# Optimization experiments

Measured on AMD Instinct MI355X. Metric: run time of the kernel, lower is better.

Reference implementation:

```python
import jax, jax.numpy as jnp
import numpy as np

LN2 = 0.6931471805599453

def ssp(x):
    # 'shifted_sp' activation: softplus(x) - log(2)
    return jax.nn.softplus(x) - LN2

def _res_chain(x, W1, b1, W2, b2):
    # PhysNetResidual chain: x <- lin2(ssp(lin1(ssp(x)))) + x
    # W1/W2: [n_res, F, F], b1/b2: [n_res, F]
    for j in range(W1.shape[0]):
        h = ssp(x) @ W1[j] + b1[j]
        x = ssp(h) @ W2[j] + b2[j] + x
    return x

def _physnet_module(feat, radial_aev, idx12, p):
    (W_I, b_I, W_J, b_J, W_gate, gvec, W_int, b_int,
     ri_W1, ri_b1, ri_W2, ri_b2,
     ra_W1, ra_b1, ra_W2, ra_b2,
     ro_W1, ro_b1, ro_W2, ro_b2, W_out, b_out) = p
    N, F = feat.shape
    # self term (no species are dummy -> non_dummy indexing is identity)
    h_self = ssp(ssp(feat) @ W_I + b_I)                       # [N,F]
    # pair messages
    gate = radial_aev @ W_gate                                 # [P,F] (no bias)
    f12 = feat[idx12]                                          # [2,P,F] gather
    fm = ssp(ssp(f12) @ W_J + b_J)                             # [2,P,F]
    pair_msg = gate[None] * fm                                 # [2,P,F]
    proto = jnp.zeros_like(feat).at[idx12.reshape(-1)].add(
        pair_msg.reshape(-1, F))                               # scatter-add
    proto = proto + h_self
    msg = _res_chain(proto, ri_W1, ri_b1, ri_W2, ri_b2)
    feat2 = feat * gvec + ssp(msg) @ W_int + b_int
    feat2 = _res_chain(feat2, ra_W1, ra_b1, ra_W2, ra_b2)
    e = ssp(_res_chain(feat2, ro_W1, ro_b1, ro_W2, ro_b2)) @ W_out + b_out  # [N]
    return e, feat2

def setup_inputs() -> dict:
    key = jax.random.key(0)
    L, F, R = 5, 128, 64
    M, A = 128, 64
    N = M * A
    P = 400000
    ks = jax.random.split(key, 20)
    s = 0.05  # small weight scale keeps activations stable across 5 modules
    inp = {
        'species': jax.random.randint(ks[0], (M, A), 0, 4, dtype=jnp.int32),
        'features': jax.random.normal(ks[1], (N, F), jnp.float32),
        'radial_aev': jax.random.uniform(ks[2], (P, R), jnp.float32),
        'atom_index12': jax.random.randint(ks[3], (2, P), 0, N, dtype=jnp.int32),
        'W_I': jax.random.normal(ks[4], (L, F, F)) * s,
        'b_I': jnp.zeros((L, F)),
        'W_J': jax.random.normal(ks[5], (L, F, F)) * s,
        'b_J': jnp.zeros((L, F)),
        'W_gate': jax.random.normal(ks[6], (L, R, F)) * s,
        'gvec': jnp.ones((L, F)),
        'W_int': jax.random.normal(ks[7], (L, F, F)) * s,
        'b_int': jnp.zeros((L, F)),
        'ri_W1': jax.random.normal(ks[8], (L, 3, F, F)) * s,
        'ri_b1': jnp.zeros((L, 3, F)),
        'ri_W2': jax.random.normal(ks[9], (L, 3, F, F)) * s,
        'ri_b2': jnp.zeros((L, 3, F)),
        'ra_W1': jax.random.normal(ks[10], (L, 2, F, F)) * s,
        'ra_b1': jnp.zeros((L, 2, F)),
        'ra_W2': jax.random.normal(ks[11], (L, 2, F, F)) * s,
        'ra_b2': jnp.zeros((L, 2, F)),
        'ro_W1': jax.random.normal(ks[12], (L, 1, F, F)) * s,
        'ro_b1': jnp.zeros((L, 1, F)),
        'ro_W2': jax.random.normal(ks[13], (L, 1, F, F)) * s,
        'ro_b2': jnp.zeros((L, 1, F)),
        'W_out': jax.random.normal(ks[14], (L, F)) * s,
        'b_out': jnp.zeros((L,)),
    }
    return inp

def reference(species, features, radial_aev, atom_index12,
              W_I, b_I, W_J, b_J, W_gate, gvec, W_int, b_int,
              ri_W1, ri_b1, ri_W2, ri_b2,
              ra_W1, ra_b1, ra_W2, ra_b2,
              ro_W1, ro_b1, ro_W2, ro_b2, W_out, b_out):
    M, A = species.shape
    params = (W_I, b_I, W_J, b_J, W_gate, gvec, W_int, b_int,
              ri_W1, ri_b1, ri_W2, ri_b2,
              ra_W1, ra_b1, ra_W2, ra_b2,
              ro_W1, ro_b1, ro_W2, ro_b2, W_out, b_out)
    feat = features
    energies = jnp.zeros((M * A,), features.dtype)
    for l in range(W_I.shape[0]):  # fixed small module loop
        p = tuple(arr[l] for arr in params)
        e, feat = _physnet_module(feat, radial_aev, atom_index12, p)
        energies = energies + e
    return energies.reshape(M, A), feat
```

## Files before the change

### kernel.cpp

```cpp
#include <hip/hip_runtime.h>


#define LN2F 0.69314718055994530942f
#define L2EF 1.44269504088896340736f
#define NB 128

using short8  = __attribute__((ext_vector_type(8))) short;
using float4v = __attribute__((ext_vector_type(4))) float;

__device__ __forceinline__ float sspf(float x) {
  float t = exp2f(-L2EF * fabsf(x));
  float l = log2f(1.0f + t);
  return fmaxf(x, 0.0f) + fmaf(LN2F, l, -LN2F);
}

__device__ __forceinline__ unsigned short f2bf(float x) {
  return (unsigned short)((__float_as_uint(x) + 0x8000u) >> 16);
}

__device__ __forceinline__ unsigned short f2bf_ne(float x) {
  unsigned int u = __float_as_uint(x);
  u += 0x7fffu + ((u >> 16) & 1u);
  return (unsigned short)(u >> 16);
}

struct K1Args {
  const float* wsrc[80];
  int isgate[80];
  const float* bp[17];
  int bstride[17];
  const float* b_out;
  const int* idx;
  unsigned short* Wt;
  float* bias_pack;
  unsigned int* H;
  int n2p, C;
};

__global__ __launch_bounds__(256) void k1_prep(K1Args K) {
  __shared__ unsigned int h[8192];
  int b = blockIdx.x, tid = threadIdx.x;
  if (b < 80) {
    const float* s = K.wsrc[b];
    unsigned short* d = K.Wt + (size_t)b * 16384;
    if (!K.isgate[b]) {
      for (int it = 0; it < 8; ++it) {
        int id = tid + it * 256;
        int lane = id & 63, mm = (id >> 6) & 3, c8 = id >> 8;
        int l16 = lane & 15, quad = lane >> 4;
        int n = 16 * c8 + l16, k0 = 8 * (4 * mm + quad);
        unsigned short tmp[8];
#pragma unroll
        for (int cc = 0; cc < 8; ++cc) tmp[cc] = f2bf_ne(s[(k0 + cc) * 128 + n]);
        *(uint4*)(d + c8 * 2048 + mm * 512 + lane * 8) = *(uint4*)tmp;
      }
    } else {
      for (int it = 0; it < 4; ++it) {
        int id = tid + it * 256;
        int lane = id & 63, mm = (id >> 6) & 1, c8 = id >> 7;
        int l16 = lane & 15, quad = lane >> 4;
        int n = 16 * c8 + l16, k0 = 8 * (4 * mm + quad);
        unsigned short tmp[8];
#pragma unroll
        for (int cc = 0; cc < 8; ++cc) tmp[cc] = f2bf_ne(s[(k0 + cc) * 128 + n]);
        *(uint4*)(d + c8 * 1024 + mm * 512 + lane * 8) = *(uint4*)tmp;
      }
    }
  } else if (b < 85) {
    int l = b - 80;
    for (int i = tid; i < 17 * 128; i += 256) {
      int s = i >> 7;
      K.bias_pack[(size_t)l * 2304 + i] = K.bp[s][l * K.bstride[s] + (i & 127)];
    }
    if (tid == 0) K.bias_pack[(size_t)l * 2304 + 17 * 128] = K.b_out[l];
  } else {
    int blk = b - 85;
    for (int i = tid; i < 8192; i += 256) h[i] = 0;
    __syncthreads();
    int s = blk * K.C, e = min(s + K.C, K.n2p);
    for (int i = s + tid; i < e; i += 256) atomicAdd(&h[K.idx[i]], 1u);
    __syncthreads();
    for (int i = tid; i < 8192; i += 256) K.H[(size_t)blk * 8192 + i] = h[i];
  }
}

__global__ __launch_bounds__(256) void col_scan(unsigned int* __restrict__ H,
                                                unsigned int* __restrict__ tot) {
  __shared__ unsigned int part[8][33];
  int c = threadIdx.x & 31, r8 = threadIdx.x >> 5;
  int col = blockIdx.x * 32 + c;
  unsigned int psum = 0;
#pragma unroll 4
  for (int r = r8 * 16; r < r8 * 16 + 16; ++r)
    psum += H[(size_t)r * 8192 + col];
  part[r8][c] = psum;
  __syncthreads();
  if (threadIdx.x < 32) {
    unsigned int run = 0;
#pragma unroll
    for (int s = 0; s < 8; ++s) {
      unsigned int v = part[s][threadIdx.x];
      part[s][threadIdx.x] = run;
      run += v;
    }
    tot[blockIdx.x * 32 + threadIdx.x] = run;
  }
  __syncthreads();
  unsigned int run = part[r8][c];
#pragma unroll 4
  for (int r = r8 * 16; r < r8 * 16 + 16; ++r) {
    unsigned int v = H[(size_t)r * 8192 + col];
    H[(size_t)r * 8192 + col] = run;
    run += v;
  }
}

__global__ __launch_bounds__(256) void place_pass(const int* __restrict__ idx,
                                                  const unsigned int* __restrict__ H,
                                                  const unsigned int* __restrict__ tot,
                                                  unsigned int* __restrict__ off_out,
                                                  unsigned int* __restrict__ pairid,
                                                  int P, int C) {
  __shared__ unsigned int pos[8192];
  __shared__ unsigned int wt4[4];
  int b = blockIdx.x, tid = threadIdx.x;
  unsigned int local[32], s = 0;
#pragma unroll
  for (int i = 0; i < 32; ++i) { local[i] = tot[tid * 32 + i]; s += local[i]; }
  unsigned int v = s;
  int lane = tid & 63, wv = tid >> 6;
#pragma unroll
  for (int o = 1; o < 64; o <<= 1) {
    unsigned int u = __shfl_up(v, o, 64);
    if (lane >= o) v += u;
  }
  if (lane == 63) wt4[wv] = v;
  __syncthreads();
  unsigned int base = 0;
  for (int k = 0; k < wv; ++k) base += wt4[k];
  unsigned int excl = base + v - s;
#pragma unroll
  for (int i = 0; i < 32; ++i) {
    pos[tid * 32 + i] = excl;
    if (b == 0) off_out[tid * 32 + i] = excl;
    excl += local[i];
  }
  if (b == 0 && tid == 255) off_out[8192] = excl;
  __syncthreads();
  for (int i = tid; i < 8192; i += 256) pos[i] += H[(size_t)b * 8192 + i];
  __syncthreads();
  int n2p = 2 * P;
  int s2 = b * C, e2 = min(s2 + C, n2p);
  for (int i = s2 + tid; i < e2; i += 256) {
    int a = idx[i];
    unsigned int p = atomicAdd(&pos[a], 1u);
    pairid[p] = (i >= P) ? (unsigned int)(i - P) : (unsigned int)i;
  }
}

__global__ __launch_bounds__(256) void gather_kernel(const float* __restrict__ radial,
                                                     const unsigned int* __restrict__ off,
                                                     const unsigned int* __restrict__ pairid,
                                                     float* __restrict__ S) {
  __shared__ float4v red[3][16];
  int a = blockIdx.x;
  int lane = threadIdx.x & 63, w = threadIdx.x >> 6;
  int grp = lane >> 4, l16v = lane & 15;
  unsigned int b = off[a], e = off[a + 1];
  float4v acc = {0.f, 0.f, 0.f, 0.f};
  for (unsigned int base = b; base < e; base += 128) {
    unsigned int pp[8];
#pragma unroll
    for (int k = 0; k < 8; ++k) {
      unsigned int j = base + k * 16 + w * 4 + grp;
      pp[k] = pairid[j < e ? j : b];
    }
    float4v vv[8];
#pragma unroll
    for (int k = 0; k < 8; ++k)
      vv[k] = *(const float4v*)(radial + (size_t)pp[k] * 64 + l16v * 4);
#pragma unroll
    for (int k = 0; k < 8; ++k) {
      unsigned int j = base + k * 16 + w * 4 + grp;
      if (j < e) acc += vv[k];
    }
  }
#pragma unroll
  for (int o = 16; o < 64; o <<= 1) {
#pragma unroll
    for (int cc = 0; cc < 4; ++cc) acc[cc] += __shfl_xor(acc[cc], o, 64);
  }
  if (w > 0 && grp == 0) red[w - 1][l16v] = acc;
  __syncthreads();
  if (w == 0 && grp == 0) {
    acc += red[0][l16v];
    acc += red[1][l16v];
    acc += red[2][l16v];
    *(float4v*)(S + (size_t)a * 64 + l16v * 4) = acc;
  }
}

struct ChainArgs {
  const float* feat_in;
  const float* S;
  const unsigned short* wt;
  const float* bias_pack;
  float* feat_out;
  float* energy;
};

#define MFMA_ __builtin_amdgcn_mfma_f32_16x16x32_bf16
#define APOFF 2176

#define BAR() { __builtin_amdgcn_sched_barrier(0); \
  asm volatile("s_waitcnt lgkmcnt(0)" ::: "memory"); \
  __builtin_amdgcn_s_barrier(); \
  __builtin_amdgcn_sched_barrier(0); }

#define LDW(WP, sp) { \
  const unsigned short* wp_ = (sp) + woff; \
  W[WP][0] = *(const short8*)(wp_); \
  W[WP][1] = *(const short8*)(wp_ + 512); \
  W[WP][2] = *(const short8*)(wp_ + 1024); \
  W[WP][3] = *(const short8*)(wp_ + 1536); }

#define BINI(ACC, B) { (ACC)[0] = (B); (ACC)[1] = (B); (ACC)[2] = (B); (ACC)[3] = (B); }

#define G128R(AP, WP, ACC) { \
  short8 a0_ = *(const short8*)(aB + (AP)*APOFF); \
  short8 a1_ = *(const short8*)(aB + (AP)*APOFF + 32); \
  short8 a2_ = *(const short8*)(aB + (AP)*APOFF + 64); \
  short8 a3_ = *(const short8*)(aB + (AP)*APOFF + 96); \
  ACC = MFMA_(a0_, W[WP][0], ACC, 0, 0, 0); \
  ACC = MFMA_(a1_, W[WP][1], ACC, 0, 0, 0); \
  ACC = MFMA_(a2_, W[WP][2], ACC, 0, 0, 0); \
  ACC = MFMA_(a3_, W[WP][3], ACC, 0, 0, 0); }

#define WSSPM(AP, V) { \
  float s0_ = sspf((V)[0]), s1_ = sspf((V)[1]); \
  float s2_ = sspf((V)[2]), s3_ = sspf((V)[3]); \
  unsigned int p01_, p23_; \
  asm("v_cvt_pk_bf16_f32 %0, %1, %2" : "=v"(p01_) : "v"(s0_), "v"(s1_)); \
  asm("v_cvt_pk_bf16_f32 %0, %1, %2" : "=v"(p23_) : "v"(s2_), "v"(s3_)); \
  wB[(AP)*APOFF]       = (unsigned short)p01_; \
  wB[(AP)*APOFF + 136] = (unsigned short)(p01_ >> 16); \
  wB[(AP)*APOFF + 272] = (unsigned short)p23_; \
  wB[(AP)*APOFF + 408] = (unsigned short)(p23_ >> 16); }

#define MODBODY(L, S0) { \
  const float* bp = A.bias_pack + (L) * 2304; \
  const unsigned short* wtp = A.wt + (size_t)(L) * 16 * 16384; \
  float bW[15]; \
  _Pragma("unroll") \
  for (int q = 0; q < 15; ++q) bW[q] = bp[q * 128 + col0]; \
  float gvv = bp[15 * 128 + col0], wvv = bp[16 * 128 + col0]; \
   \
  { LDW((S0)^1, wtp + 2*16384); \
    gG = Z; \
    { short8 s0_ = *(const short8*)(aS); short8 s1_ = *(const short8*)(aS + 32); \
      gG = MFMA_(s0_, GT0, gG, 0, 0, 0); \
      gG = MFMA_(s1_, GT1, gG, 0, 0, 0); } \
    BINI(fm, bW[0]); G128R(0, (S0), fm); \
    for (int r = 0; r < 4; ++r) fm[r] = sspf(fm[r]); } \
   \
  { LDW((S0), wtp + 3*16384); \
    if ((L) < 4) { \
      GT0 = *(const short8*)(wtp + 16*16384 + goff); \
      GT1 = *(const short8*)(wtp + 16*16384 + goff + 512); \
    } \
    BINI(t4, bW[1]); G128R(0, (S0)^1, t4); \
    for (int r = 0; r < 4; ++r) xf[r] = fm[r] * gG[r] + sspf(t4[r]); } \
  WSSPM(1, xf); BAR(); \
   \
  { LDW((S0)^1, wtp + 4*16384); BINI(t4, bW[2]); G128R(1, (S0), t4); } \
  WSSPM(0, t4); BAR(); \
  { LDW((S0), wtp + 5*16384); BINI(t4, bW[3]); G128R(0, (S0)^1, t4); \
    for (int r = 0; r < 4; ++r) xf[r] += t4[r]; } \
  WSSPM(1, xf); BAR(); \
  { LDW((S0)^1, wtp + 6*16384); BINI(t4, bW[4]); G128R(1, (S0), t4); } \
  WSSPM(0, t4); BAR(); \
  { LDW((S0), wtp + 7*16384); BINI(t4, bW[5]); G128R(0, (S0)^1, t4); \
    for (int r = 0; r < 4; ++r) xf[r] += t4[r]; } \
  WSSPM(1, xf); BAR(); \
  { LDW((S0)^1, wtp + 8*16384); BINI(t4, bW[6]); G128R(1, (S0), t4); } \
  WSSPM(0, t4); BAR(); \
  { LDW((S0), wtp + 9*16384); BINI(t4, bW[7]); G128R(0, (S0)^1, t4); \
    for (int r = 0; r < 4; ++r) xf[r] += t4[r]; } \
  WSSPM(1, xf); BAR(); \
   \
  { LDW((S0)^1, wtp + 10*16384); BINI(t4, bW[8]); G128R(1, (S0), t4); \
    for (int r = 0; r < 4; ++r) xf[r] = ff[r] * gvv + t4[r]; } \
  WSSPM(0, xf); BAR(); \
   \
  { LDW((S0), wtp + 11*16384); BINI(t4, bW[9]); G128R(0, (S0)^1, t4); } \
  WSSPM(1, t4); BAR(); \
  { LDW((S0)^1, wtp + 12*16384); BINI(t4, bW[10]); G128R(1, (S0), t4); \
    for (int r = 0; r < 4; ++r) xf[r] += t4[r]; } \
  WSSPM(0, xf); BAR(); \
  { LDW((S0), wtp + 13*16384); BINI(t4, bW[11]); G128R(0, (S0)^1, t4); } \
  WSSPM(1, t4); BAR(); \
  { LDW((S0)^1, wtp + 14*16384); BINI(t4, bW[12]); G128R(1, (S0), t4); \
    for (int r = 0; r < 4; ++r) xf[r] += t4[r]; } \
  WSSPM(0, xf); BAR(); \
  ff = xf; \
  if ((L) == 4) { \
    for (int r = 0; r < 4; ++r) \
      A.feat_out[(size_t)(row0 + quad*4 + r) * 128 + col0] = xf[r]; \
  } \
   \
  { LDW((S0), wtp + 15*16384); BINI(t4, bW[13]); G128R(0, (S0)^1, t4); } \
  WSSPM(1, t4); BAR(); \
   \
  { if ((L) < 4) LDW((S0)^1, wtp + 17*16384); \
    BINI(t4, bW[14]); G128R(1, (S0), t4); \
    p0 += sspf(xf[0] + t4[0]) * wvv; \
    p1 += sspf(xf[1] + t4[1]) * wvv; \
    p2 += sspf(xf[2] + t4[2]) * wvv; \
    p3 += sspf(xf[3] + t4[3]) * wvv; } \
  bsum += bp[17*128]; \
  BAR(); }

__global__ __launch_bounds__(512)
__attribute__((amdgpu_waves_per_eu(4, 4)))
void chain_kernel(ChainArgs A) {
  __shared__ __align__(16) unsigned short sA[2][16 * 136];
  __shared__ __align__(16) unsigned short sS[16 * 72];
  __shared__ float sE[16];

  const int tid  = threadIdx.x;
  const int row0 = blockIdx.x * 16;
  const int lane = tid & 63;
  const int c    = tid >> 6;
  const int l16  = lane & 15;
  const int quad = lane >> 4;
  const int col0 = 16 * c + l16;

  const int woff = c * 2048 + lane * 8;
  const int goff = c * 1024 + lane * 8;

  const unsigned short* aB = &sA[0][0] + l16 * 136 + quad * 8;
  unsigned short*       wB = &sA[0][0] + (quad * 4) * 136 + col0;
  const unsigned short* aS = &sS[0] + l16 * 72 + quad * 8;

  short8 GT0, GT1;
  short8 W[2][4];
  GT0 = *(const short8*)(A.wt + goff);
  GT1 = *(const short8*)(A.wt + goff + 512);
  LDW(0, A.wt + 16384);

  for (int i = tid; i < 16 * 64; i += 512) {
    int r = i >> 6, k = i & 63;
    sS[r * 72 + k] = f2bf(A.S[(size_t)(row0 + r) * 64 + k]);
  }
  for (int i = tid; i < 16 * 128; i += 512) {
    int r = i >> 7, k = i & 127;
    sA[0][r * 136 + k] = f2bf(sspf(A.feat_in[(size_t)(row0 + r) * 128 + k]));
  }
  float4v ff;
#pragma unroll
  for (int r = 0; r < 4; ++r)
    ff[r] = A.feat_in[(size_t)(row0 + quad * 4 + r) * 128 + col0];
  if (tid < 16) sE[tid] = 0.0f;
  __syncthreads();

  const float4v Z = {0.f, 0.f, 0.f, 0.f};
  float4v gG, fm, xf, t4;
  float p0 = 0.f, p1 = 0.f, p2 = 0.f, p3 = 0.f, bsum = 0.f;

  MODBODY(0, 0)
  MODBODY(1, 1)
  MODBODY(2, 0)
  MODBODY(3, 1)
  MODBODY(4, 0)

#pragma unroll
  for (int o = 1; o < 16; o <<= 1) {
    p0 += __shfl_xor(p0, o, 64);
    p1 += __shfl_xor(p1, o, 64);
    p2 += __shfl_xor(p2, o, 64);
    p3 += __shfl_xor(p3, o, 64);
  }
  if (l16 == 0) {
    atomicAdd(&sE[quad * 4 + 0], p0);
    atomicAdd(&sE[quad * 4 + 1], p1);
    atomicAdd(&sE[quad * 4 + 2], p2);
    atomicAdd(&sE[quad * 4 + 3], p3);
  }
  BAR();
  if (tid < 16) A.energy[row0 + tid] = sE[tid] + bsum;
}

extern "C" void kernel_launch(void* const* d_in, const int* in_sizes, int n_in,
                              void* d_out, int out_size, void* d_ws, size_t ws_size,
                              hipStream_t stream) {
  const float* features = (const float*)d_in[1];
  const float* radial   = (const float*)d_in[2];
  const int*   idx12    = (const int*)  d_in[3];
  const float* W_I    = (const float*)d_in[4];
  const float* b_I    = (const float*)d_in[5];
  const float* W_J    = (const float*)d_in[6];
  const float* b_J    = (const float*)d_in[7];
  const float* W_gate = (const float*)d_in[8];
  const float* gvec   = (const float*)d_in[9];
  const float* W_int  = (const float*)d_in[10];
  const float* b_int  = (const float*)d_in[11];
  const float* ri_W1  = (const float*)d_in[12];
  const float* ri_b1  = (const float*)d_in[13];
  const float* ri_W2  = (const float*)d_in[14];
  const float* ri_b2  = (const float*)d_in[15];
  const float* ra_W1  = (const float*)d_in[16];
  const float* ra_b1  = (const float*)d_in[17];
  const float* ra_W2  = (const float*)d_in[18];
  const float* ra_b2  = (const float*)d_in[19];
  const float* ro_W1  = (const float*)d_in[20];
  const float* ro_b1  = (const float*)d_in[21];
  const float* ro_W2  = (const float*)d_in[22];
  const float* ro_b2  = (const float*)d_in[23];
  const float* W_out  = (const float*)d_in[24];
  const float* b_out  = (const float*)d_in[25];

  const int N = in_sizes[1] / 128;
  const int P = in_sizes[3] / 2;
  const int L = in_sizes[25];
  const int n2p = 2 * P;
  const int C = (n2p + NB - 1) / NB;

  float* S = (float*)d_ws;
  float* bias_pack = S + (size_t)N * 64;
  unsigned short* Wt = (unsigned short*)(bias_pack + 5 * 2304);
  unsigned int* H      = (unsigned int*)(Wt + (size_t)80 * 16384);
  unsigned int* tot    = H + (size_t)NB * 8192;
  unsigned int* off    = tot + N;
  unsigned int* pairid = off + N + 4;

  K1Args k1;
  for (int l = 0; l < L; ++l) {
    const float* fx[16] = {
      W_gate + l * 8192,
      W_J + l * 16384, W_I + l * 16384,
      ri_W1 + (l * 3 + 0) * 16384, ri_W2 + (l * 3 + 0) * 16384,
      ri_W1 + (l * 3 + 1) * 16384, ri_W2 + (l * 3 + 1) * 16384,
      ri_W1 + (l * 3 + 2) * 16384, ri_W2 + (l * 3 + 2) * 16384,
      W_int + l * 16384,
      ra_W1 + (l * 2 + 0) * 16384, ra_W2 + (l * 2 + 0) * 16384,
      ra_W1 + (l * 2 + 1) * 16384, ra_W2 + (l * 2 + 1) * 16384,
      ro_W1 + l * 16384, ro_W2 + l * 16384 };
    for (int t = 0; t < 16; ++t) { k1.wsrc[l * 16 + t] = fx[t]; k1.isgate[l * 16 + t] = (t == 0); }
  }
  const float* bp[17] = { b_J, b_I,
    ri_b1, ri_b2, ri_b1 + 128, ri_b2 + 128, ri_b1 + 256, ri_b2 + 256,
    b_int, ra_b1, ra_b2, ra_b1 + 128, ra_b2 + 128, ro_b1, ro_b2, gvec, W_out };
  int st[17] = {128,128, 384,384,384,384,384,384, 128, 256,256,256,256, 128,128,128,128};
  for (int q = 0; q < 17; ++q) { k1.bp[q] = bp[q]; k1.bstride[q] = st[q]; }
  k1.b_out = b_out;
  k1.idx = idx12; k1.Wt = Wt; k1.bias_pack = bias_pack; k1.H = H;
  k1.n2p = n2p; k1.C = C;
  k1_prep<<<80 + 5 + NB, 256, 0, stream>>>(k1);

  col_scan<<<256, 256, 0, stream>>>(H, tot);
  place_pass<<<NB, 256, 0, stream>>>(idx12, H, tot, off, pairid, P, C);
  gather_kernel<<<N, 256, 0, stream>>>(radial, off, pairid, S);

  ChainArgs ca;
  ca.feat_in   = features;
  ca.S         = S;
  ca.wt        = Wt;
  ca.bias_pack = bias_pack;
  ca.energy    = (float*)d_out;
  ca.feat_out  = (float*)d_out + N;
  chain_kernel<<<N / 16, 512, 0, stream>>>(ca);
}
```

Baseline: 318.8 us.

## Process 32 rows per block in chain kernel to reuse weight registers

Each block of the chain kernel now handles two 16-row tiles instead of one. Every weight fragment loaded from global memory feeds two interleaved MFMA accumulators, which halves weight traffic per row and gives independent MFMA chains for latency hiding. The cost is double the LDS activation buffers, more registers per thread, waves-per-EU lowered from 4 to 2, and half as many blocks (256 instead of 512), which may underfill the GPU.

Result: slower. 327.1 us (+2.6%).

```diff
diff --git a/kernel.cpp b/kernel.cpp
--- a/kernel.cpp
+++ b/kernel.cpp
@@ -210,7 +210,8 @@
 };
 
 #define MFMA_ __builtin_amdgcn_mfma_f32_16x16x32_bf16
-#define APOFF 2176
+#define APOFF 4352
+#define TOFF  2176
 
 #define BAR() { __builtin_amdgcn_sched_barrier(0); \
   asm volatile("s_waitcnt lgkmcnt(0)" ::: "memory"); \
@@ -226,26 +227,36 @@
 
 #define BINI(ACC, B) { (ACC)[0] = (B); (ACC)[1] = (B); (ACC)[2] = (B); (ACC)[3] = (B); }
 
-#define G128R(AP, WP, ACC) { \
+#define G128R2(AP, WP, ACC0, ACC1) { \
   short8 a0_ = *(const short8*)(aB + (AP)*APOFF); \
   short8 a1_ = *(const short8*)(aB + (AP)*APOFF + 32); \
   short8 a2_ = *(const short8*)(aB + (AP)*APOFF + 64); \
   short8 a3_ = *(const short8*)(aB + (AP)*APOFF + 96); \
-  ACC = MFMA_(a0_, W[WP][0], ACC, 0, 0, 0); \
-  ACC = MFMA_(a1_, W[WP][1], ACC, 0, 0, 0); \
-  ACC = MFMA_(a2_, W[WP][2], ACC, 0, 0, 0); \
-  ACC = MFMA_(a3_, W[WP][3], ACC, 0, 0, 0); }
-
-#define WSSPM(AP, V) { \
+  short8 c0_ = *(const short8*)(aB2 + (AP)*APOFF); \
+  short8 c1_ = *(const short8*)(aB2 + (AP)*APOFF + 32); \
+  short8 c2_ = *(const short8*)(aB2 + (AP)*APOFF + 64); \
+  short8 c3_ = *(const short8*)(aB2 + (AP)*APOFF + 96); \
+  ACC0 = MFMA_(a0_, W[WP][0], ACC0, 0, 0, 0); \
+  ACC1 = MFMA_(c0_, W[WP][0], ACC1, 0, 0, 0); \
+  ACC0 = MFMA_(a1_, W[WP][1], ACC0, 0, 0, 0); \
+  ACC1 = MFMA_(c1_, W[WP][1], ACC1, 0, 0, 0); \
+  ACC0 = MFMA_(a2_, W[WP][2], ACC0, 0, 0, 0); \
+  ACC1 = MFMA_(c2_, W[WP][2], ACC1, 0, 0, 0); \
+  ACC0 = MFMA_(a3_, W[WP][3], ACC0, 0, 0, 0); \
+  ACC1 = MFMA_(c3_, W[WP][3], ACC1, 0, 0, 0); }
+
+#define WSSP_P(PTR, AP, V) { \
   float s0_ = sspf((V)[0]), s1_ = sspf((V)[1]); \
   float s2_ = sspf((V)[2]), s3_ = sspf((V)[3]); \
   unsigned int p01_, p23_; \
   asm("v_cvt_pk_bf16_f32 %0, %1, %2" : "=v"(p01_) : "v"(s0_), "v"(s1_)); \
   asm("v_cvt_pk_bf16_f32 %0, %1, %2" : "=v"(p23_) : "v"(s2_), "v"(s3_)); \
-  wB[(AP)*APOFF]       = (unsigned short)p01_; \
-  wB[(AP)*APOFF + 136] = (unsigned short)(p01_ >> 16); \
-  wB[(AP)*APOFF + 272] = (unsigned short)p23_; \
-  wB[(AP)*APOFF + 408] = (unsigned short)(p23_ >> 16); }
+  (PTR)[(AP)*APOFF]       = (unsigned short)p01_; \
+  (PTR)[(AP)*APOFF + 136] = (unsigned short)(p01_ >> 16); \
+  (PTR)[(AP)*APOFF + 272] = (unsigned short)p23_; \
+  (PTR)[(AP)*APOFF + 408] = (unsigned short)(p23_ >> 16); }
+
+#define WSSPM2(AP, V0, V1) { WSSP_P(wB, AP, V0); WSSP_P(wB2, AP, V1); }
 
 #define MODBODY(L, S0) { \
   const float* bp = A.bias_pack + (L) * 2304; \
@@ -256,79 +267,111 @@
   float gvv = bp[15 * 128 + col0], wvv = bp[16 * 128 + col0]; \
    \
   { LDW((S0)^1, wtp + 2*16384); \
-    gG = Z; \
+    gG0 = Z; gG1 = Z; \
     { short8 s0_ = *(const short8*)(aS); short8 s1_ = *(const short8*)(aS + 32); \
-      gG = MFMA_(s0_, GT0, gG, 0, 0, 0); \
-      gG = MFMA_(s1_, GT1, gG, 0, 0, 0); } \
-    BINI(fm, bW[0]); G128R(0, (S0), fm); \
-    for (int r = 0; r < 4; ++r) fm[r] = sspf(fm[r]); } \
+      short8 s2_ = *(const short8*)(aS2); short8 s3_ = *(const short8*)(aS2 + 32); \
+      gG0 = MFMA_(s0_, GT0, gG0, 0, 0, 0); \
+      gG1 = MFMA_(s2_, GT0, gG1, 0, 0, 0); \
+      gG0 = MFMA_(s1_, GT1, gG0, 0, 0, 0); \
+      gG1 = MFMA_(s3_, GT1, gG1, 0, 0, 0); } \
+    BINI(fm0, bW[0]); BINI(fm1, bW[0]); \
+    G128R2(0, (S0), fm0, fm1); \
+    for (int r = 0; r < 4; ++r) fm0[r] = sspf(fm0[r]); \
+    for (int r = 0; r < 4; ++r) fm1[r] = sspf(fm1[r]); } \
    \
   { LDW((S0), wtp + 3*16384); \
     if ((L) < 4) { \
       GT0 = *(const short8*)(wtp + 16*16384 + goff); \
       GT1 = *(const short8*)(wtp + 16*16384 + goff + 512); \
     } \
-    BINI(t4, bW[1]); G128R(0, (S0)^1, t4); \
-    for (int r = 0; r < 4; ++r) xf[r] = fm[r] * gG[r] + sspf(t4[r]); } \
-  WSSPM(1, xf); BAR(); \
-   \
-  { LDW((S0)^1, wtp + 4*16384); BINI(t4, bW[2]); G128R(1, (S0), t4); } \
-  WSSPM(0, t4); BAR(); \
-  { LDW((S0), wtp + 5*16384); BINI(t4, bW[3]); G128R(0, (S0)^1, t4); \
-    for (int r = 0; r < 4; ++r) xf[r] += t4[r]; } \
-  WSSPM(1, xf); BAR(); \
-  { LDW((S0)^1, wtp + 6*16384); BINI(t4, bW[4]); G128R(1, (S0), t4); } \
-  WSSPM(0, t4); BAR(); \
-  { LDW((S0), wtp + 7*16384); BINI(t4, bW[5]); G128R(0, (S0)^1, t4); \
-    for (int r = 0; r < 4; ++r) xf[r] += t4[r]; } \
-  WSSPM(1, xf); BAR(); \
-  { LDW((S0)^1, wtp + 8*16384); BINI(t4, bW[6]); G128R(1, (S0), t4); } \
-  WSSPM(0, t4); BAR(); \
-  { LDW((S0), wtp + 9*16384); BINI(t4, bW[7]); G128R(0, (S0)^1, t4); \
-    for (int r = 0; r < 4; ++r) xf[r] += t4[r]; } \
-  WSSPM(1, xf); BAR(); \
-   \
-  { LDW((S0)^1, wtp + 10*16384); BINI(t4, bW[8]); G128R(1, (S0), t4); \
-    for (int r = 0; r < 4; ++r) xf[r] = ff[r] * gvv + t4[r]; } \
-  WSSPM(0, xf); BAR(); \
-   \
-  { LDW((S0), wtp + 11*16384); BINI(t4, bW[9]); G128R(0, (S0)^1, t4); } \
-  WSSPM(1, t4); BAR(); \
-  { LDW((S0)^1, wtp + 12*16384); BINI(t4, bW[10]); G128R(1, (S0), t4); \
-    for (int r = 0; r < 4; ++r) xf[r] += t4[r]; } \
-  WSSPM(0, xf); BAR(); \
-  { LDW((S0), wtp + 13*16384); BINI(t4, bW[11]); G128R(0, (S0)^1, t4); } \
-  WSSPM(1, t4); BAR(); \
-  { LDW((S0)^1, wtp + 14*16384); BINI(t4, bW[12]); G128R(1, (S0), t4); \
-    for (int r = 0; r < 4; ++r) xf[r] += t4[r]; } \
-  WSSPM(0, xf); BAR(); \
-  ff = xf; \
+    BINI(t40, bW[1]); BINI(t41, bW[1]); \
+    G128R2(0, (S0)^1, t40, t41); \
+    for (int r = 0; r < 4; ++r) xf0[r] = fm0[r] * gG0[r] + sspf(t40[r]); \
+    for (int r = 0; r < 4; ++r) xf1[r] = fm1[r] * gG1[r] + sspf(t41[r]); } \
+  WSSPM2(1, xf0, xf1); BAR(); \
+   \
+  { LDW((S0)^1, wtp + 4*16384); BINI(t40, bW[2]); BINI(t41, bW[2]); \
+    G128R2(1, (S0), t40, t41); } \
+  WSSPM2(0, t40, t41); BAR(); \
+  { LDW((S0), wtp + 5*16384); BINI(t40, bW[3]); BINI(t41, bW[3]); \
+    G128R2(0, (S0)^1, t40, t41); \
+    for (int r = 0; r < 4; ++r) xf0[r] += t40[r]; \
+    for (int r = 0; r < 4; ++r) xf1[r] += t41[r]; } \
+  WSSPM2(1, xf0, xf1); BAR(); \
+  { LDW((S0)^1, wtp + 6*16384); BINI(t40, bW[4]); BINI(t41, bW[4]); \
+    G128R2(1, (S0), t40, t41); } \
+  WSSPM2(0, t40, t41); BAR(); \
+  { LDW((S0), wtp + 7*16384); BINI(t40, bW[5]); BINI(t41, bW[5]); \
+    G128R2(0, (S0)^1, t40, t41); \
+    for (int r = 0; r < 4; ++r) xf0[r] += t40[r]; \
+    for (int r = 0; r < 4; ++r) xf1[r] += t41[r]; } \
+  WSSPM2(1, xf0, xf1); BAR(); \
+  { LDW((S0)^1, wtp + 8*16384); BINI(t40, bW[6]); BINI(t41, bW[6]); \
+    G128R2(1, (S0), t40, t41); } \
+  WSSPM2(0, t40, t41); BAR(); \
+  { LDW((S0), wtp + 9*16384); BINI(t40, bW[7]); BINI(t41, bW[7]); \
+    G128R2(0, (S0)^1, t40, t41); \
+    for (int r = 0; r < 4; ++r) xf0[r] += t40[r]; \
+    for (int r = 0; r < 4; ++r) xf1[r] += t41[r]; } \
+  WSSPM2(1, xf0, xf1); BAR(); \
+   \
+  { LDW((S0)^1, wtp + 10*16384); BINI(t40, bW[8]); BINI(t41, bW[8]); \
+    G128R2(1, (S0), t40, t41); \
+    for (int r = 0; r < 4; ++r) xf0[r] = ff0[r] * gvv + t40[r]; \
+    for (int r = 0; r < 4; ++r) xf1[r] = ff1[r] * gvv + t41[r]; } \
+  WSSPM2(0, xf0, xf1); BAR(); \
+   \
+  { LDW((S0), wtp + 11*16384); BINI(t40, bW[9]); BINI(t41, bW[9]); \
+    G128R2(0, (S0)^1, t40, t41); } \
+  WSSPM2(1, t40, t41); BAR(); \
+  { LDW((S0)^1, wtp + 12*16384); BINI(t40, bW[10]); BINI(t41, bW[10]); \
+    G128R2(1, (S0), t40, t41); \
+    for (int r = 0; r < 4; ++r) xf0[r] += t40[r]; \
+    for (int r = 0; r < 4; ++r) xf1[r] += t41[r]; } \
+  WSSPM2(0, xf0, xf1); BAR(); \
+  { LDW((S0), wtp + 13*16384); BINI(t40, bW[11]); BINI(t41, bW[11]); \
+    G128R2(0, (S0)^1, t40, t41); } \
+  WSSPM2(1, t40, t41); BAR(); \
+  { LDW((S0)^1, wtp + 14*16384); BINI(t40, bW[12]); BINI(t41, bW[12]); \
+    G128R2(1, (S0), t40, t41); \
+    for (int r = 0; r < 4; ++r) xf0[r] += t40[r]; \
+    for (int r = 0; r < 4; ++r) xf1[r] += t41[r]; } \
+  WSSPM2(0, xf0, xf1); BAR(); \
+  ff0 = xf0; ff1 = xf1; \
   if ((L) == 4) { \
     for (int r = 0; r < 4; ++r) \
-      A.feat_out[(size_t)(row0 + quad*4 + r) * 128 + col0] = xf[r]; \
+      A.feat_out[(size_t)(row0 + quad*4 + r) * 128 + col0] = xf0[r]; \
+    for (int r = 0; r < 4; ++r) \
+      A.feat_out[(size_t)(row0 + 16 + quad*4 + r) * 128 + col0] = xf1[r]; \
   } \
    \
-  { LDW((S0), wtp + 15*16384); BINI(t4, bW[13]); G128R(0, (S0)^1, t4); } \
-  WSSPM(1, t4); BAR(); \
+  { LDW((S0), wtp + 15*16384); BINI(t40, bW[13]); BINI(t41, bW[13]); \
+    G128R2(0, (S0)^1, t40, t41); } \
+  WSSPM2(1, t40, t41); BAR(); \
    \
   { if ((L) < 4) LDW((S0)^1, wtp + 17*16384); \
-    BINI(t4, bW[14]); G128R(1, (S0), t4); \
-    p0 += sspf(xf[0] + t4[0]) * wvv; \
-    p1 += sspf(xf[1] + t4[1]) * wvv; \
-    p2 += sspf(xf[2] + t4[2]) * wvv; \
-    p3 += sspf(xf[3] + t4[3]) * wvv; } \
+    BINI(t40, bW[14]); BINI(t41, bW[14]); \
+    G128R2(1, (S0), t40, t41); \
+    p0 += sspf(xf0[0] + t40[0]) * wvv; \
+    p1 += sspf(xf0[1] + t40[1]) * wvv; \
+    p2 += sspf(xf0[2] + t40[2]) * wvv; \
+    p3 += sspf(xf0[3] + t40[3]) * wvv; \
+    p4 += sspf(xf1[0] + t41[0]) * wvv; \
+    p5 += sspf(xf1[1] + t41[1]) * wvv; \
+    p6 += sspf(xf1[2] + t41[2]) * wvv; \
+    p7 += sspf(xf1[3] + t41[3]) * wvv; } \
   bsum += bp[17*128]; \
   BAR(); }
 
 __global__ __launch_bounds__(512)
-__attribute__((amdgpu_waves_per_eu(4, 4)))
+__attribute__((amdgpu_waves_per_eu(2, 2)))
 void chain_kernel(ChainArgs A) {
-  __shared__ __align__(16) unsigned short sA[2][16 * 136];
-  __shared__ __align__(16) unsigned short sS[16 * 72];
-  __shared__ float sE[16];
+  __shared__ __align__(16) unsigned short sA[2][32 * 136];
+  __shared__ __align__(16) unsigned short sS[32 * 72];
+  __shared__ float sE[32];
 
   const int tid  = threadIdx.x;
-  const int row0 = blockIdx.x * 16;
+  const int row0 = blockIdx.x * 32;
   const int lane = tid & 63;
   const int c    = tid >> 6;
   const int l16  = lane & 15;
@@ -338,9 +381,12 @@
   const int woff = c * 2048 + lane * 8;
   const int goff = c * 1024 + lane * 8;
 
-  const unsigned short* aB = &sA[0][0] + l16 * 136 + quad * 8;
-  unsigned short*       wB = &sA[0][0] + (quad * 4) * 136 + col0;
-  const unsigned short* aS = &sS[0] + l16 * 72 + quad * 8;
+  const unsigned short* aB  = &sA[0][0] + l16 * 136 + quad * 8;
+  const unsigned short* aB2 = aB + TOFF;
+  unsigned short*       wB  = &sA[0][0] + (quad * 4) * 136 + col0;
+  unsigned short*       wB2 = wB + TOFF;
+  const unsigned short* aS  = &sS[0] + l16 * 72 + quad * 8;
+  const unsigned short* aS2 = aS + 16 * 72;
 
   short8 GT0, GT1;
   short8 W[2][4];
@@ -348,24 +394,27 @@
   GT1 = *(const short8*)(A.wt + goff + 512);
   LDW(0, A.wt + 16384);
 
-  for (int i = tid; i < 16 * 64; i += 512) {
+  for (int i = tid; i < 32 * 64; i += 512) {
     int r = i >> 6, k = i & 63;
     sS[r * 72 + k] = f2bf(A.S[(size_t)(row0 + r) * 64 + k]);
   }
-  for (int i = tid; i < 16 * 128; i += 512) {
+  for (int i = tid; i < 32 * 128; i += 512) {
     int r = i >> 7, k = i & 127;
     sA[0][r * 136 + k] = f2bf(sspf(A.feat_in[(size_t)(row0 + r) * 128 + k]));
   }
-  float4v ff;
-#pragma unroll
-  for (int r = 0; r < 4; ++r)
-    ff[r] = A.feat_in[(size_t)(row0 + quad * 4 + r) * 128 + col0];
-  if (tid < 16) sE[tid] = 0.0f;
+  float4v ff0, ff1;
+#pragma unroll
+  for (int r = 0; r < 4; ++r) {
+    ff0[r] = A.feat_in[(size_t)(row0 + quad * 4 + r) * 128 + col0];
+    ff1[r] = A.feat_in[(size_t)(row0 + 16 + quad * 4 + r) * 128 + col0];
+  }
+  if (tid < 32) sE[tid] = 0.0f;
   __syncthreads();
 
   const float4v Z = {0.f, 0.f, 0.f, 0.f};
-  float4v gG, fm, xf, t4;
-  float p0 = 0.f, p1 = 0.f, p2 = 0.f, p3 = 0.f, bsum = 0.f;
+  float4v gG0, gG1, fm0, fm1, xf0, xf1, t40, t41;
+  float p0 = 0.f, p1 = 0.f, p2 = 0.f, p3 = 0.f;
+  float p4 = 0.f, p5 = 0.f, p6 = 0.f, p7 = 0.f, bsum = 0.f;
 
   MODBODY(0, 0)
   MODBODY(1, 1)
@@ -379,15 +428,23 @@
     p1 += __shfl_xor(p1, o, 64);
     p2 += __shfl_xor(p2, o, 64);
     p3 += __shfl_xor(p3, o, 64);
+    p4 += __shfl_xor(p4, o, 64);
+    p5 += __shfl_xor(p5, o, 64);
+    p6 += __shfl_xor(p6, o, 64);
+    p7 += __shfl_xor(p7, o, 64);
   }
   if (l16 == 0) {
     atomicAdd(&sE[quad * 4 + 0], p0);
     atomicAdd(&sE[quad * 4 + 1], p1);
     atomicAdd(&sE[quad * 4 + 2], p2);
     atomicAdd(&sE[quad * 4 + 3], p3);
+    atomicAdd(&sE[16 + quad * 4 + 0], p4);
+    atomicAdd(&sE[16 + quad * 4 + 1], p5);
+    atomicAdd(&sE[16 + quad * 4 + 2], p6);
+    atomicAdd(&sE[16 + quad * 4 + 3], p7);
   }
   BAR();
-  if (tid < 16) A.energy[row0 + tid] = sE[tid] + bsum;
+  if (tid < 32) A.energy[row0 + tid] = sE[tid] + bsum;
 }
 
 extern "C" void kernel_launch(void* const* d_in, const int* in_sizes, int n_in,
@@ -468,5 +525,5 @@
   ca.bias_pack = bias_pack;
   ca.energy    = (float*)d_out;
   ca.feat_out  = (float*)d_out + N;
-  chain_kernel<<<N / 16, 512, 0, stream>>>(ca);
-}
+  chain_kernel<<<N / 32, 512, 0, stream>>>(ca);
+}
```
